# Kernel optimization log

Hardware: AMD Instinct MI355X
Metric: run time of the kernel (lower is better)

Reference implementation:

```python
import jax, jax.numpy as jnp
import numpy as np

N_QUBITS = 11
N_CIRCUITS = 3
N_ROTS = 6
BATCH = 512
C64 = jnp.complex64


def _ry_mat(theta):
    # RY(t) = [[cos t/2, -sin t/2], [sin t/2, cos t/2]]
    c = jnp.cos(theta * 0.5)
    s = jnp.sin(theta * 0.5)
    return jnp.stack([jnp.stack([c, -s]), jnp.stack([s, c])]).astype(C64)


def _rz_mat(theta):
    # RZ(t) = diag(e^{-i t/2}, e^{+i t/2})
    e = jnp.exp((-0.5j) * theta.astype(C64))
    z = jnp.zeros_like(e)
    return jnp.stack([jnp.stack([e, z]), jnp.stack([z, jnp.conj(e)])])


def _apply_1q(state, U, q):
    # state: (2,)*n complex; apply 2x2 U on axis q (PennyLane wire q = axis q)
    out = jnp.tensordot(U, state, axes=((1,), (q,)))
    return jnp.moveaxis(out, 0, q)


def _apply_ctrl(state, U, c, t):
    # controlled-U on wires [c(control), t(target)]: block_diag(I2, U) in |c t> basis
    U4 = jnp.eye(4, dtype=C64).at[2:, 2:].set(U)
    out = jnp.tensordot(U4.reshape(2, 2, 2, 2), state, axes=((2, 3), (c, t)))
    return jnp.moveaxis(out, (0, 1), (c, t))


def _simulate(angles):
    # angles: [n_circuits, 6, n_qubits] -> expvals [2*n_qubits] (X then Z)
    n = N_QUBITS
    state = jnp.zeros((2,) * n, dtype=C64).at[(0,) * n].set(1.0)
    for i in range(N_CIRCUITS):
        for q in range(n):
            state = _apply_1q(state, _ry_mat(angles[i, 0, q]), q)
            state = _apply_1q(state, _rz_mat(angles[i, 1, q]), q)
            state = _apply_1q(state, _ry_mat(angles[i, 2, q]), q)
            state = _apply_1q(state, _rz_mat(angles[i, 3, q]), q)
        for q in range(n):
            t = (q + 1) % n
            state = _apply_ctrl(state, _ry_mat(angles[i, 4, q]), q, t)
            state = _apply_ctrl(state, _rz_mat(angles[i, 5, q]), q, t)
    ex_x, ex_z = [], []
    for q in range(n):
        s0 = jnp.take(state, 0, axis=q)
        s1 = jnp.take(state, 1, axis=q)
        # <X_q> = 2 Re <psi_{q=0}|psi_{q=1}>,  <Z_q> = p(q=0) - p(q=1)
        ex_x.append(2.0 * jnp.real(jnp.vdot(s0, s1)))
        ex_z.append(jnp.sum(jnp.abs(s0) ** 2 - jnp.abs(s1) ** 2))
    return jnp.stack(ex_x + ex_z).astype(jnp.float32)


def setup_inputs() -> dict:
    key = jax.random.key(0)
    k1, k2, k3 = jax.random.split(key, 3)
    x = jax.random.normal(k1, (BATCH, N_QUBITS), dtype=jnp.float32)
    W = jax.random.uniform(k2, (N_CIRCUITS, N_QUBITS * N_ROTS, N_QUBITS),
                           dtype=jnp.float32, minval=-0.01, maxval=0.01)
    b = jax.random.uniform(k3, (N_CIRCUITS, N_QUBITS * N_ROTS),
                           dtype=jnp.float32, minval=-0.01, maxval=0.01)
    return {"x": x, "W": W, "b": b}


def reference(x, W, b):
    # per-circuit Linear (dropout is identity in eval): [B, C, n_rots*n_qubits]
    rot = jnp.einsum('coi,bi->bco', W, x) + b[None, :, :]
    angles = rot.reshape(x.shape[0], N_CIRCUITS, N_ROTS, N_QUBITS)
    return jax.vmap(_simulate)(angles)  # [B, 2*n_qubits]
```

## Files before the change

kernel.cpp:

```cpp
#include <hip/hip_runtime.h>

#define NQ 11
#define NC 3
#define NANG (NC * 66)
#define BLOCK 512

typedef float f2 __attribute__((ext_vector_type(2)));

__device__ __forceinline__ f2 swp(f2 v) { return __builtin_shufflevector(v, v, 1, 0); }

template<int CTRL>
__device__ __forceinline__ float dppx(float v) {
  return __int_as_float(__builtin_amdgcn_update_dpp(
      0, __float_as_int(v), CTRL, 0xF, 0xF, false));
}
template<int CTRL>
__device__ __forceinline__ f2 dpp2(f2 v) {
  f2 r; r.x = dppx<CTRL>(v.x); r.y = dppx<CTRL>(v.y); return r;
}
__device__ __forceinline__ f2 shfl2(f2 v, int m) {
  f2 r; r.x = __shfl_xor(v.x, m, 64); r.y = __shfl_xor(v.y, m, 64); return r;
}
__device__ __forceinline__ float plp16(float v, int lane) {
  auto r = __builtin_amdgcn_permlane16_swap(__float_as_int(v), __float_as_int(v), false, false);
  return __int_as_float((lane & 16) ? r[0] : r[1]);
}
__device__ __forceinline__ float plp32(float v, int lane) {
  auto r = __builtin_amdgcn_permlane32_swap(__float_as_int(v), __float_as_int(v), false, false);
  return __int_as_float((lane & 32) ? r[0] : r[1]);
}
__device__ __forceinline__ f2 plp16_2(f2 v, int lane) {
  f2 r; r.x = plp16(v.x, lane); r.y = plp16(v.y, lane); return r;
}
__device__ __forceinline__ f2 plp32_2(f2 v, int lane) {
  f2 r; r.x = plp32(v.x, lane); r.y = plp32(v.y, lane); return r;
}
__device__ __forceinline__ float plsum16(float v) {
  auto r = __builtin_amdgcn_permlane16_swap(__float_as_int(v), __float_as_int(v), false, false);
  return __int_as_float(r[0]) + __int_as_float(r[1]);
}
__device__ __forceinline__ float plsum32(float v) {
  auto r = __builtin_amdgcn_permlane32_swap(__float_as_int(v), __float_as_int(v), false, false);
  return __int_as_float(r[0]) + __int_as_float(r[1]);
}

__device__ __forceinline__ void apply2p(f2& v0, f2& v1, float4 U) {
  const f2 ai2 = {-U.y, U.y};
  const f2 bi2 = {-U.w, U.w};
  const f2 w0 = swp(v0), w1 = swp(v1);
  const f2 n0 =  U.x * v0 + ai2 * w0 + U.z * v1 + bi2 * w1;
  const f2 n1 = -U.z * v0 + bi2 * w0 + U.x * v1 - ai2 * w1;
  v0 = n0; v1 = n1;
}
__device__ __forceinline__ void gpartp(f2& v, f2 p, float4 U, bool hi) {
  const f2 ai2 = hi ? f2{U.y, -U.y} : f2{-U.y, U.y};
  const float br = hi ? -U.z : U.z;
  const f2 bi2 = {-U.w, U.w};
  v = U.x * v + ai2 * swp(v) + br * p + bi2 * swp(p);
}

template<int M>
__device__ __forceinline__ void g_shfl(f2 (&s)[4], float4 U, int lane) {
  const bool hi = (lane & M) != 0;
#pragma unroll
  for (int i = 0; i < 4; ++i) gpartp(s[i], shfl2(s[i], M), U, hi);
}
template<int CTRL, int M>
__device__ __forceinline__ void g_dpp(f2 (&s)[4], float4 U, int lane) {
  const bool hi = (lane & M) != 0;
#pragma unroll
  for (int i = 0; i < 4; ++i) gpartp(s[i], dpp2<CTRL>(s[i]), U, hi);
}
__device__ __forceinline__ void g_pl16(f2 (&s)[4], float4 U, int lane) {
  const bool hi = (lane & 16) != 0;
#pragma unroll
  for (int i = 0; i < 4; ++i) gpartp(s[i], plp16_2(s[i], lane), U, hi);
}
__device__ __forceinline__ void g_pl32_regsel(f2 (&s)[4], float4 U0, float4 U1, int lane) {
  const bool hi = (lane & 32) != 0;
#pragma unroll
  for (int i = 0; i < 4; ++i)
    gpartp(s[i], plp32_2(s[i], lane), (i & 1) ? U1 : U0, hi);
}
template<int WVX>
__device__ __forceinline__ void g_wave(f2 (&s)[4], float4 U, f2* buf, int wave, int lane) {
  const int base = (wave << 6) | lane;
#pragma unroll
  for (int i = 0; i < 4; ++i) buf[(i << 9) | base] = s[i];
  __syncthreads();
  const int pbase = ((wave ^ WVX) << 6) | lane;
  const bool hi = (wave & WVX) != 0;
#pragma unroll
  for (int i = 0; i < 4; ++i) gpartp(s[i], buf[(i << 9) | pbase], U, hi);
}

__global__ __launch_bounds__(BLOCK) void qsim_kernel(
    const float* __restrict__ x, const float* __restrict__ W,
    const float* __restrict__ bias, float* __restrict__ out) {
  const int bidx = blockIdx.x;
  const int tid = threadIdx.x;
  const int lane = tid & 63, wave = tid >> 6;

  __shared__ float xs[NQ];
  __shared__ float ang[NANG];
  __shared__ float4 m1s[NC * NQ];
  __shared__ float4 m2s[NC * NQ];
  __shared__ float4 v1s[NC * 10];
  __shared__ f2 ex0[2048];
  __shared__ f2 ex1[2048];
  __shared__ float red[8][24];

  if (tid < NQ) xs[tid] = x[bidx * NQ + tid];
  __syncthreads();

  if (tid < NANG) {
    const int c = tid / 66, o = tid - c * 66;
    const float* wr = W + (c * 66 + o) * NQ;
    float s = bias[c * 66 + o];
#pragma unroll
    for (int i = 0; i < NQ; ++i) s += wr[i] * xs[i];
    ang[tid] = s;
  }
  __syncthreads();

  if (tid < 2 * NC * NQ) {
    const int kind = tid / (NC * NQ);
    const int id = tid - kind * (NC * NQ);
    const int c = id / NQ, q = id - c * NQ;
    const float* a = ang + c * 66;
    if (kind == 0) {
      float s0,c0,s1,c1,s2,c2,s3,c3;
      sincosf(0.5f*a[q],      &s0,&c0);
      sincosf(0.5f*a[11+q],   &s1,&c1);
      sincosf(0.5f*a[22+q],   &s2,&c2);
      sincosf(0.5f*a[33+q],   &s3,&c3);
      const float mar = c1*c0, mai = -s1*c0;
      const float mbr = -c1*s0, mbi = s1*s0;
      const float nar = c2*mar + s2*mbr, nai = c2*mai - s2*mbi;
      const float nbr = c2*mbr - s2*mar, nbi = c2*mbi + s2*mai;
      m1s[id] = make_float4(c3*nar + s3*nai, c3*nai - s3*nar,
                            c3*nbr + s3*nbi, c3*nbi - s3*nbr);
    } else {
      float s4,c4,s5,c5;
      sincosf(0.5f*a[44+q], &s4,&c4);
      sincosf(0.5f*a[55+q], &s5,&c5);
      m2s[id] = make_float4(c5*c4, -s5*c4, -c5*s4, s5*s4);
    }
  }
  __syncthreads();

  if (tid < NC * 10) {
    const int c = tid / 10, tt = tid - c * 10, t = tt + 1;
    const float4 A = m2s[c*NQ + t - 1];
    const float4 B = m1s[c*NQ + t];
    const float pr_=A.x, pi_=A.y, qr_=A.z, qi_=A.w;
    const float ar_=B.x, ai_=B.y, br_=B.z, bi_=B.w;
    v1s[c*10 + tt] = make_float4(
      (pr_*ar_ - pi_*ai_) - (qr_*br_ + qi_*bi_),
      (pr_*ai_ + pi_*ar_) - (qi_*br_ - qr_*bi_),
      (pr_*br_ - pi_*bi_) + (qr_*ar_ + qi_*ai_),
      (pr_*bi_ + pi_*br_) + (qi_*ar_ - qr_*ai_));
  }
  __syncthreads();

  f2 s[4];
#pragma unroll
  for (int i = 0; i < 4; ++i) s[i] = f2{0.f, 0.f};
  if (tid == 0) s[0].x = 1.f;

  int par = 0;
  for (int c = 0; c < NC; ++c) {
    const float4* M1 = &m1s[c * NQ];
    const float4* VF = &v1s[c * 10];
    {
      const float4 U = M1[0];
      apply2p(s[0], s[1], U);
      apply2p(s[2], s[3], U);
    }
    g_pl32_regsel(s, M1[1], VF[0], lane);
    g_pl16(s, *((lane & 32) ? &VF[1] : &M1[2]), lane);
    g_shfl<8>(s, *((lane & 16) ? &VF[2] : &M1[3]), lane);
    g_wave<4>(s, *((lane & 8) ? &VF[3] : &M1[4]),
              par ? ex1 : ex0, wave, lane); par ^= 1;
    g_wave<2>(s, *((wave & 4) ? &VF[4] : &M1[5]),
              par ? ex1 : ex0, wave, lane); par ^= 1;
    g_wave<1>(s, *((wave & 2) ? &VF[5] : &M1[6]),
              par ? ex1 : ex0, wave, lane); par ^= 1;
    g_shfl<4>(s, *((wave & 1) ? &VF[6] : &M1[7]), lane);
    g_dpp<0x4E,2>(s, *((lane & 4) ? &VF[7] : &M1[8]), lane);
    g_dpp<0xB1,1>(s, *((lane & 2) ? &VF[8] : &M1[9]), lane);
    {
      const float4 U = *((lane & 1) ? &VF[9] : &M1[10]);
      apply2p(s[0], s[2], U);
      apply2p(s[1], s[3], U);
    }
    {
      const float4 U = m2s[c * NQ + 10];
      apply2p(s[2], s[3], U);
    }
  }

  f2* eb = par ? ex1 : ex0;
  const int base = (wave << 6) | lane;
#pragma unroll
  for (int i = 0; i < 4; ++i) eb[(i << 9) | base] = s[i];
  __syncthreads();
  const int pb4 = ((wave ^ 4) << 6) | lane;
  const int pb2 = ((wave ^ 2) << 6) | lane;
  const int pb1 = ((wave ^ 1) << 6) | lane;
  f2 aq4 = {0,0}, aq5 = {0,0}, aq6 = {0,0};
#pragma unroll
  for (int i = 0; i < 4; ++i) {
    aq4 += s[i] * eb[(i << 9) | pb4];
    aq5 += s[i] * eb[(i << 9) | pb2];
    aq6 += s[i] * eb[(i << 9) | pb1];
  }
  f2 mg[4];
#pragma unroll
  for (int i = 0; i < 4; ++i) mg[i] = s[i] * s[i];
  const f2 ztv  = (mg[0] + mg[1]) + (mg[2] + mg[3]);
  const f2 z0v  = (mg[0] - mg[1]) + (mg[2] - mg[3]);
  const f2 z10v = (mg[0] + mg[1]) - (mg[2] + mg[3]);
  f2 aq0={0,0}, aq10={0,0}, aq9={0,0}, aq8={0,0}, aq7={0,0}, aq3={0,0}, aq2={0,0}, aq1={0,0};
#pragma unroll
  for (int i = 0; i < 4; ++i) {
    aq0  += s[i] * s[i ^ 1];
    aq10 += s[i] * s[i ^ 2];
    aq9  += s[i] * dpp2<0xB1>(s[i]);
    aq8  += s[i] * dpp2<0x4E>(s[i]);
    aq7  += s[i] * shfl2(s[i], 4);
    aq3  += s[i] * shfl2(s[i], 8);
    aq2  += s[i] * plp16_2(s[i], lane);
    aq1  += s[i] * plp32_2(s[i], lane);
  }
  const float ztot = ztv.x + ztv.y;

  float v[22];
  v[0]=aq0.x+aq0.y; v[1]=aq1.x+aq1.y; v[2]=aq2.x+aq2.y; v[3]=aq3.x+aq3.y;
  v[4]=aq4.x+aq4.y; v[5]=aq5.x+aq5.y; v[6]=aq6.x+aq6.y;
  v[7]=aq7.x+aq7.y; v[8]=aq8.x+aq8.y; v[9]=aq9.x+aq9.y; v[10]=aq10.x+aq10.y;
  v[11] = z0v.x + z0v.y;
  v[12] = (lane & 32) ? -ztot : ztot;
  v[13] = (lane & 16) ? -ztot : ztot;
  v[14] = (lane & 8)  ? -ztot : ztot;
  v[15] = (wave & 4)  ? -ztot : ztot;
  v[16] = (wave & 2)  ? -ztot : ztot;
  v[17] = (wave & 1)  ? -ztot : ztot;
  v[18] = (lane & 4)  ? -ztot : ztot;
  v[19] = (lane & 2)  ? -ztot : ztot;
  v[20] = (lane & 1)  ? -ztot : ztot;
  v[21] = z10v.x + z10v.y;

#pragma unroll
  for (int k = 0; k < 22; ++k) {
    v[k] += dppx<0xB1>(v[k]);
    v[k] += dppx<0x4E>(v[k]);
  }
  const int q4l = lane & 3;
  float wv[6];
#pragma unroll
  for (int p = 0; p < 5; ++p)
    wv[p] = q4l == 0 ? v[4*p] : (q4l == 1 ? v[4*p+1] : (q4l == 2 ? v[4*p+2] : v[4*p+3]));
  wv[5] = q4l == 0 ? v[20] : (q4l == 1 ? v[21] : 0.f);
#pragma unroll
  for (int p = 0; p < 6; ++p) {
    wv[p] += __shfl_xor(wv[p], 4, 64);
    wv[p] += __shfl_xor(wv[p], 8, 64);
    wv[p] = plsum16(wv[p]);
    wv[p] = plsum32(wv[p]);
  }
  if (lane < 4) {
#pragma unroll
    for (int p = 0; p < 6; ++p) red[wave][4*p + lane] = wv[p];
  }
  __syncthreads();
  if (tid < 22) {
    float sacc = 0.f;
#pragma unroll
    for (int w8 = 0; w8 < 8; ++w8) sacc += red[w8][tid];
    out[bidx * 22 + tid] = sacc;
  }
}

extern "C" void kernel_launch(void* const* d_in, const int* in_sizes, int n_in,
                              void* d_out, int out_size, void* d_ws, size_t ws_size,
                              hipStream_t stream) {
  (void)n_in; (void)d_ws; (void)ws_size; (void)out_size;
  const float* x = (const float*)d_in[0];
  const float* W = (const float*)d_in[1];
  const float* b = (const float*)d_in[2];
  float* out = (float*)d_out;
  const int batch = in_sizes[0] / NQ;
  qsim_kernel<<<batch, BLOCK, 0, stream>>>(x, W, b, out);
}
```

Baseline: 21.59 us.

## Switch statevector registers from interleaved complex to split real/imag layout

Each thread's four amplitudes were stored as interleaved (re,im) pairs. They now live in split real/imag f2 vectors, where each f2 pairs the two amplitudes of the lowest qubit. Gate math becomes broadcast-scalar times vector, which can map to packed FMA without the swizzles the old complex multiply needed. Qubit 10 now acts within the vector through swaps, and the measurement reductions are rewritten for this layout. The risk is extra swap and select work on the last-qubit gates and a different register allocation.

After: 23.40 us. 8.4% more time.

```diff
diff --git a/kernel.cpp b/kernel.cpp
--- a/kernel.cpp
+++ b/kernel.cpp
@@ -7,6 +7,7 @@
 
 typedef float f2 __attribute__((ext_vector_type(2)));
 
+__device__ __forceinline__ f2 bc(float v) { return f2{v, v}; }
 __device__ __forceinline__ f2 swp(f2 v) { return __builtin_shufflevector(v, v, 1, 0); }
 
 template<int CTRL>
@@ -44,54 +45,26 @@
   return __int_as_float(r[0]) + __int_as_float(r[1]);
 }
 
-__device__ __forceinline__ void apply2p(f2& v0, f2& v1, float4 U) {
-  const f2 ai2 = {-U.y, U.y};
-  const f2 bi2 = {-U.w, U.w};
-  const f2 w0 = swp(v0), w1 = swp(v1);
-  const f2 n0 =  U.x * v0 + ai2 * w0 + U.z * v1 + bi2 * w1;
-  const f2 n1 = -U.z * v0 + bi2 * w0 + U.x * v1 - ai2 * w1;
-  v0 = n0; v1 = n1;
-}
-__device__ __forceinline__ void gpartp(f2& v, f2 p, float4 U, bool hi) {
-  const f2 ai2 = hi ? f2{U.y, -U.y} : f2{-U.y, U.y};
-  const float br = hi ? -U.z : U.z;
-  const f2 bi2 = {-U.w, U.w};
-  v = U.x * v + ai2 * swp(v) + br * p + bi2 * swp(p);
-}
-
-template<int M>
-__device__ __forceinline__ void g_shfl(f2 (&s)[4], float4 U, int lane) {
-  const bool hi = (lane & M) != 0;
-#pragma unroll
-  for (int i = 0; i < 4; ++i) gpartp(s[i], shfl2(s[i], M), U, hi);
-}
-template<int CTRL, int M>
-__device__ __forceinline__ void g_dpp(f2 (&s)[4], float4 U, int lane) {
-  const bool hi = (lane & M) != 0;
-#pragma unroll
-  for (int i = 0; i < 4; ++i) gpartp(s[i], dpp2<CTRL>(s[i]), U, hi);
-}
-__device__ __forceinline__ void g_pl16(f2 (&s)[4], float4 U, int lane) {
-  const bool hi = (lane & 16) != 0;
-#pragma unroll
-  for (int i = 0; i < 4; ++i) gpartp(s[i], plp16_2(s[i], lane), U, hi);
-}
-__device__ __forceinline__ void g_pl32_regsel(f2 (&s)[4], float4 U0, float4 U1, int lane) {
-  const bool hi = (lane & 32) != 0;
-#pragma unroll
-  for (int i = 0; i < 4; ++i)
-    gpartp(s[i], plp32_2(s[i], lane), (i & 1) ? U1 : U0, hi);
-}
+__device__ __forceinline__ void prow(f2& r, f2& i, f2 pr, f2 pi,
+                                     float ar, float ai2, float br2, float bi) {
+  const f2 nr = bc(ar)*r - bc(ai2)*i + bc(br2)*pr - bc(bi)*pi;
+  const f2 ni = bc(ar)*i + bc(ai2)*r + bc(br2)*pi + bc(bi)*pr;
+  r = nr; i = ni;
+}
+__device__ __forceinline__ void gcross(f2& r, f2& i, f2 pr, f2 pi, float4 U, bool hi) {
+  prow(r, i, pr, pi, U.x, hi ? -U.y : U.y, hi ? -U.z : U.z, U.w);
+}
+
 template<int WVX>
-__device__ __forceinline__ void g_wave(f2 (&s)[4], float4 U, f2* buf, int wave, int lane) {
+__device__ __forceinline__ void g_wave(f2& Ar, f2& Ai, f2& Br, f2& Bi, float4 U,
+                                       f2* __restrict__ buf, int wave, int lane) {
   const int base = (wave << 6) | lane;
-#pragma unroll
-  for (int i = 0; i < 4; ++i) buf[(i << 9) | base] = s[i];
-  __syncthreads();
-  const int pbase = ((wave ^ WVX) << 6) | lane;
+  buf[base] = Ar; buf[512 + base] = Ai; buf[1024 + base] = Br; buf[1536 + base] = Bi;
+  __syncthreads();
+  const int pb = ((wave ^ WVX) << 6) | lane;
   const bool hi = (wave & WVX) != 0;
-#pragma unroll
-  for (int i = 0; i < 4; ++i) gpartp(s[i], buf[(i << 9) | pbase], U, hi);
+  gcross(Ar, Ai, buf[pb],        buf[512 + pb],  U, hi);
+  gcross(Br, Bi, buf[1024 + pb], buf[1536 + pb], U, hi);
 }
 
 __global__ __launch_bounds__(BLOCK) void qsim_kernel(
@@ -163,10 +136,8 @@
   }
   __syncthreads();
 
-  f2 s[4];
-#pragma unroll
-  for (int i = 0; i < 4; ++i) s[i] = f2{0.f, 0.f};
-  if (tid == 0) s[0].x = 1.f;
+  f2 Ar = {0,0}, Ai = {0,0}, Br = {0,0}, Bi = {0,0};
+  if (tid == 0) Ar.x = 1.f;
 
   int par = 0;
   for (int c = 0; c < NC; ++c) {
@@ -174,72 +145,123 @@
     const float4* VF = &v1s[c * 10];
     {
       const float4 U = M1[0];
-      apply2p(s[0], s[1], U);
-      apply2p(s[2], s[3], U);
-    }
-    g_pl32_regsel(s, M1[1], VF[0], lane);
-    g_pl16(s, *((lane & 32) ? &VF[1] : &M1[2]), lane);
-    g_shfl<8>(s, *((lane & 16) ? &VF[2] : &M1[3]), lane);
-    g_wave<4>(s, *((lane & 8) ? &VF[3] : &M1[4]),
-              par ? ex1 : ex0, wave, lane); par ^= 1;
-    g_wave<2>(s, *((wave & 4) ? &VF[4] : &M1[5]),
-              par ? ex1 : ex0, wave, lane); par ^= 1;
-    g_wave<1>(s, *((wave & 2) ? &VF[5] : &M1[6]),
-              par ? ex1 : ex0, wave, lane); par ^= 1;
-    g_shfl<4>(s, *((wave & 1) ? &VF[6] : &M1[7]), lane);
-    g_dpp<0x4E,2>(s, *((lane & 4) ? &VF[7] : &M1[8]), lane);
-    g_dpp<0xB1,1>(s, *((lane & 2) ? &VF[8] : &M1[9]), lane);
+      const f2 oAr = Ar, oAi = Ai;
+      prow(Ar, Ai, Br, Bi,  U.x,  U.y,  U.z, U.w);
+      prow(Br, Bi, oAr, oAi, U.x, -U.y, -U.z, U.w);
+    }
+    {
+      const float4 U0 = M1[1], U1 = VF[0];
+      const bool hi = (lane & 32) != 0;
+      gcross(Ar, Ai, plp32_2(Ar,lane), plp32_2(Ai,lane), U0, hi);
+      gcross(Br, Bi, plp32_2(Br,lane), plp32_2(Bi,lane), U1, hi);
+    }
+    {
+      const float4 U = *((lane & 32) ? &VF[1] : &M1[2]);
+      const bool hi = (lane & 16) != 0;
+      gcross(Ar, Ai, plp16_2(Ar,lane), plp16_2(Ai,lane), U, hi);
+      gcross(Br, Bi, plp16_2(Br,lane), plp16_2(Bi,lane), U, hi);
+    }
+    {
+      const float4 U = *((lane & 16) ? &VF[2] : &M1[3]);
+      const bool hi = (lane & 8) != 0;
+      gcross(Ar, Ai, shfl2(Ar,8), shfl2(Ai,8), U, hi);
+      gcross(Br, Bi, shfl2(Br,8), shfl2(Bi,8), U, hi);
+    }
+    g_wave<4>(Ar,Ai,Br,Bi, *((lane & 8) ? &VF[3] : &M1[4]), par ? ex1 : ex0, wave, lane); par ^= 1;
+    g_wave<2>(Ar,Ai,Br,Bi, *((wave & 4) ? &VF[4] : &M1[5]), par ? ex1 : ex0, wave, lane); par ^= 1;
+    g_wave<1>(Ar,Ai,Br,Bi, *((wave & 2) ? &VF[5] : &M1[6]), par ? ex1 : ex0, wave, lane); par ^= 1;
+    {
+      const float4 U = *((wave & 1) ? &VF[6] : &M1[7]);
+      const bool hi = (lane & 4) != 0;
+      gcross(Ar, Ai, shfl2(Ar,4), shfl2(Ai,4), U, hi);
+      gcross(Br, Bi, shfl2(Br,4), shfl2(Bi,4), U, hi);
+    }
+    {
+      const float4 U = *((lane & 4) ? &VF[7] : &M1[8]);
+      const bool hi = (lane & 2) != 0;
+      gcross(Ar, Ai, dpp2<0x4E>(Ar), dpp2<0x4E>(Ai), U, hi);
+      gcross(Br, Bi, dpp2<0x4E>(Br), dpp2<0x4E>(Bi), U, hi);
+    }
+    {
+      const float4 U = *((lane & 2) ? &VF[8] : &M1[9]);
+      const bool hi = (lane & 1) != 0;
+      gcross(Ar, Ai, dpp2<0xB1>(Ar), dpp2<0xB1>(Ai), U, hi);
+      gcross(Br, Bi, dpp2<0xB1>(Br), dpp2<0xB1>(Bi), U, hi);
+    }
     {
       const float4 U = *((lane & 1) ? &VF[9] : &M1[10]);
-      apply2p(s[0], s[2], U);
-      apply2p(s[1], s[3], U);
+      const f2 vai = f2{-U.y, U.y};
+      const f2 vbr = f2{U.z, -U.z};
+      {
+        const f2 sr = swp(Ar), si = swp(Ai);
+        const f2 nr = bc(U.x)*Ar + vai*Ai + vbr*sr - bc(U.w)*si;
+        const f2 ni = bc(U.x)*Ai - vai*Ar + vbr*si + bc(U.w)*sr;
+        Ar = nr; Ai = ni;
+      }
+      {
+        const f2 sr = swp(Br), si = swp(Bi);
+        const f2 nr = bc(U.x)*Br + vai*Bi + vbr*sr - bc(U.w)*si;
+        const f2 ni = bc(U.x)*Bi - vai*Br + vbr*si + bc(U.w)*sr;
+        Br = nr; Bi = ni;
+      }
     }
     {
       const float4 U = m2s[c * NQ + 10];
-      apply2p(s[2], s[3], U);
+      const f2 ma  = f2{1.f, U.x};
+      const f2 mai = f2{0.f, U.y};
+      const f2 mbr = f2{0.f, U.z};
+      const f2 mbi = f2{0.f, U.w};
+      const f2 oAr = Ar, oAi = Ai;
+      const f2 nAr = ma*Ar - mai*Ai + mbr*Br - mbi*Bi;
+      const f2 nAi = ma*Ai + mai*Ar + mbr*Bi + mbi*Br;
+      const f2 nBr = ma*Br + mai*Bi - mbr*oAr - mbi*oAi;
+      const f2 nBi = ma*Bi - mai*Br - mbr*oAi + mbi*oAr;
+      Ar = nAr; Ai = nAi; Br = nBr; Bi = nBi;
     }
   }
 
   f2* eb = par ? ex1 : ex0;
   const int base = (wave << 6) | lane;
-#pragma unroll
-  for (int i = 0; i < 4; ++i) eb[(i << 9) | base] = s[i];
+  eb[base] = Ar; eb[512 + base] = Ai; eb[1024 + base] = Br; eb[1536 + base] = Bi;
   __syncthreads();
   const int pb4 = ((wave ^ 4) << 6) | lane;
   const int pb2 = ((wave ^ 2) << 6) | lane;
   const int pb1 = ((wave ^ 1) << 6) | lane;
-  f2 aq4 = {0,0}, aq5 = {0,0}, aq6 = {0,0};
-#pragma unroll
-  for (int i = 0; i < 4; ++i) {
-    aq4 += s[i] * eb[(i << 9) | pb4];
-    aq5 += s[i] * eb[(i << 9) | pb2];
-    aq6 += s[i] * eb[(i << 9) | pb1];
-  }
-  f2 mg[4];
-#pragma unroll
-  for (int i = 0; i < 4; ++i) mg[i] = s[i] * s[i];
-  const f2 ztv  = (mg[0] + mg[1]) + (mg[2] + mg[3]);
-  const f2 z0v  = (mg[0] - mg[1]) + (mg[2] - mg[3]);
-  const f2 z10v = (mg[0] + mg[1]) - (mg[2] + mg[3]);
-  f2 aq0={0,0}, aq10={0,0}, aq9={0,0}, aq8={0,0}, aq7={0,0}, aq3={0,0}, aq2={0,0}, aq1={0,0};
-#pragma unroll
-  for (int i = 0; i < 4; ++i) {
-    aq0  += s[i] * s[i ^ 1];
-    aq10 += s[i] * s[i ^ 2];
-    aq9  += s[i] * dpp2<0xB1>(s[i]);
-    aq8  += s[i] * dpp2<0x4E>(s[i]);
-    aq7  += s[i] * shfl2(s[i], 4);
-    aq3  += s[i] * shfl2(s[i], 8);
-    aq2  += s[i] * plp16_2(s[i], lane);
-    aq1  += s[i] * plp32_2(s[i], lane);
-  }
-  const float ztot = ztv.x + ztv.y;
+  f2 t;
+  t = Ar*eb[pb4] + Ai*eb[512+pb4] + Br*eb[1024+pb4] + Bi*eb[1536+pb4];
+  const float xq4 = t.x + t.y;
+  t = Ar*eb[pb2] + Ai*eb[512+pb2] + Br*eb[1024+pb2] + Bi*eb[1536+pb2];
+  const float xq5 = t.x + t.y;
+  t = Ar*eb[pb1] + Ai*eb[512+pb1] + Br*eb[1024+pb1] + Bi*eb[1536+pb1];
+  const float xq6 = t.x + t.y;
+
+  const f2 mgA = Ar*Ar + Ai*Ai;
+  const f2 mgB = Br*Br + Bi*Bi;
+  const f2 mgS = mgA + mgB;
+  const float ztot = mgS.x + mgS.y;
+  const float zq0  = (mgA.x + mgA.y) - (mgB.x + mgB.y);
+  const float zq10 = mgS.x - mgS.y;
+  t = Ar*Br + Ai*Bi;
+  const float xq0 = 2.f * (t.x + t.y);
+  t = Ar*swp(Ar) + Ai*swp(Ai) + Br*swp(Br) + Bi*swp(Bi);
+  const float xq10 = t.x + t.y;
+  t = Ar*dpp2<0xB1>(Ar) + Ai*dpp2<0xB1>(Ai) + Br*dpp2<0xB1>(Br) + Bi*dpp2<0xB1>(Bi);
+  const float xq9 = t.x + t.y;
+  t = Ar*dpp2<0x4E>(Ar) + Ai*dpp2<0x4E>(Ai) + Br*dpp2<0x4E>(Br) + Bi*dpp2<0x4E>(Bi);
+  const float xq8 = t.x + t.y;
+  t = Ar*shfl2(Ar,4) + Ai*shfl2(Ai,4) + Br*shfl2(Br,4) + Bi*shfl2(Bi,4);
+  const float xq7 = t.x + t.y;
+  t = Ar*shfl2(Ar,8) + Ai*shfl2(Ai,8) + Br*shfl2(Br,8) + Bi*shfl2(Bi,8);
+  const float xq3 = t.x + t.y;
+  t = Ar*plp16_2(Ar,lane) + Ai*plp16_2(Ai,lane) + Br*plp16_2(Br,lane) + Bi*plp16_2(Bi,lane);
+  const float xq2 = t.x + t.y;
+  t = Ar*plp32_2(Ar,lane) + Ai*plp32_2(Ai,lane) + Br*plp32_2(Br,lane) + Bi*plp32_2(Bi,lane);
+  const float xq1 = t.x + t.y;
 
   float v[22];
-  v[0]=aq0.x+aq0.y; v[1]=aq1.x+aq1.y; v[2]=aq2.x+aq2.y; v[3]=aq3.x+aq3.y;
-  v[4]=aq4.x+aq4.y; v[5]=aq5.x+aq5.y; v[6]=aq6.x+aq6.y;
-  v[7]=aq7.x+aq7.y; v[8]=aq8.x+aq8.y; v[9]=aq9.x+aq9.y; v[10]=aq10.x+aq10.y;
-  v[11] = z0v.x + z0v.y;
+  v[0]=xq0; v[1]=xq1; v[2]=xq2; v[3]=xq3; v[4]=xq4; v[5]=xq5; v[6]=xq6;
+  v[7]=xq7; v[8]=xq8; v[9]=xq9; v[10]=xq10;
+  v[11] = zq0;
   v[12] = (lane & 32) ? -ztot : ztot;
   v[13] = (lane & 16) ? -ztot : ztot;
   v[14] = (lane & 8)  ? -ztot : ztot;
@@ -249,7 +271,7 @@
   v[18] = (lane & 4)  ? -ztot : ztot;
   v[19] = (lane & 2)  ? -ztot : ztot;
   v[20] = (lane & 1)  ? -ztot : ztot;
-  v[21] = z10v.x + z10v.y;
+  v[21] = zq10;
 
 #pragma unroll
   for (int k = 0; k < 22; ++k) {
```
